# Optimization experiments

Measured on AMD Instinct MI355X. Metric: run time of the kernel, lower is better.

Reference implementation:

```python
import jax, jax.numpy as jnp
import numpy as np

N_NODES = 50000
N_EDGES = 800000
EDGE_DIM = 64
HID = 64


def setup_inputs() -> dict:
    key = jax.random.key(0)
    ks = jax.random.split(key, 8)
    hidden_atom_emb = jax.random.normal(ks[0], (N_NODES, HID), dtype=jnp.float32)
    edge_emb = jax.random.normal(ks[1], (N_EDGES, EDGE_DIM), dtype=jnp.float32)
    edge_list = jax.random.randint(ks[2], (N_EDGES, 2), 0, N_NODES, dtype=jnp.int64)
    # filter MLP params (xavier-uniform-like scaling)
    lim1 = float(np.sqrt(6.0 / (EDGE_DIM + HID)))
    W1 = jax.random.uniform(ks[3], (EDGE_DIM, HID), minval=-lim1, maxval=lim1, dtype=jnp.float32)
    b1 = jnp.zeros((HID,), dtype=jnp.float32)
    lim2 = float(np.sqrt(6.0 / (HID + HID)))
    W2 = jax.random.uniform(ks[4], (HID, HID), minval=-lim2, maxval=lim2, dtype=jnp.float32)
    b2 = jnp.zeros((HID,), dtype=jnp.float32)
    lim3 = 1.414 * float(np.sqrt(6.0 / (HID + 1)))
    linear_coef = jax.random.uniform(ks[5], (HID, 1), minval=-lim3, maxval=lim3, dtype=jnp.float32)
    return {
        'hidden_atom_emb': hidden_atom_emb,
        'edge_emb': edge_emb,
        'W1': W1, 'b1': b1, 'W2': W2, 'b2': b2,
        'linear_coef': linear_coef,
        'edge_list': edge_list,
    }


def reference(hidden_atom_emb, edge_emb, W1, b1, W2, b2, linear_coef, edge_list):
    # filter-generating MLP: Linear + tanh, Linear
    hidden_edge_emb = jnp.tanh(edge_emb @ W1 + b1) @ W2 + b2            # [E, H]
    # gather neighbor (source) embeddings and apply continuous filter
    msg = hidden_atom_emb[edge_list[:, 1]] * hidden_edge_emb           # [E, H]
    # unnormalized edge attention (scalar per edge)
    attn = jnp.exp(msg @ linear_coef)                                   # [E, 1]
    dest = edge_list[:, 0]
    n = hidden_atom_emb.shape[0]
    # scatter-sum over neighbors (dim=1 of the sparse [N,N,H] tensors)
    num = jax.ops.segment_sum(msg * attn, dest, num_segments=n)         # [N, H]
    den = jax.ops.segment_sum(jnp.broadcast_to(attn, msg.shape), dest, num_segments=n)  # [N, H]
    return jnp.where(den > 0, num / den, num)
```

## Files before the change

kernel.cpp:

```cpp
#include <hip/hip_runtime.h>
#include <math.h>


#define TE 64
#define HID 64

typedef __attribute__((ext_vector_type(8))) short short8;
typedef __attribute__((ext_vector_type(4))) float float4v;

__device__ __forceinline__ float fast_tanh(float x) {
    float t = __expf(2.0f * x);
    return 1.0f - 2.0f * __builtin_amdgcn_rcpf(t + 1.0f);
}

__device__ __forceinline__ void split_bf16(float x, unsigned short& hi,
                                           unsigned short& lo) {
    unsigned b = __float_as_uint(x);
    hi = (unsigned short)(b >> 16);
    float hf = __uint_as_float(b & 0xffff0000u);
    lo = (unsigned short)(__float_as_uint(x - hf) >> 16);
}

__global__ __launch_bounds__(256) void pack_w(
    const float* __restrict__ W1, const float* __restrict__ W2,
    unsigned short* __restrict__ wpack)
{
    int t = threadIdx.x;
    for (int i = 0; i < 16; ++i) {
        int idx = t * 16 + i;
        int k = idx >> 6, f = idx & 63;
        int nt = f >> 4, n = f & 15, ks = k >> 5, q = (k >> 3) & 3, j = k & 7;
        int fi = (((nt * 2 + ks) * 4 + q) * 16 + n) * 8 + j;
        unsigned short hi, lo;
        split_bf16(W1[idx], hi, lo);
        wpack[fi] = hi; wpack[4096 + fi] = lo;
        split_bf16(W2[idx], hi, lo);
        wpack[8192 + fi] = hi; wpack[12288 + fi] = lo;
    }
}


__global__ __launch_bounds__(256) void hist_kernel(
    const int2* __restrict__ edge_list, int* __restrict__ cursor, int E)
{
    int i = blockIdx.x * blockDim.x + threadIdx.x;
    if (i < E) atomicAdd(&cursor[edge_list[i].x], 1);
}

__global__ __launch_bounds__(1024) void scanA_kernel(
    int* __restrict__ a, int* __restrict__ blocksums, int N)
{
    __shared__ int wsum[16];
    const int t = threadIdx.x;
    const int lane = t & 63, wv = t >> 6;
    int i = blockIdx.x * 1024 + t;
    int x = (i < N) ? a[i] : 0;
    int v = x;
    #pragma unroll
    for (int d = 1; d < 64; d <<= 1) {
        int y = __shfl_up(v, d);
        if (lane >= d) v += y;
    }
    if (lane == 63) wsum[wv] = v;
    __syncthreads();
    if (wv == 0 && lane < 16) {
        int s = wsum[lane];
        #pragma unroll
        for (int d = 1; d < 16; d <<= 1) {
            int y = __shfl_up(s, d);
            if (lane >= d) s += y;
        }
        wsum[lane] = s;
    }
    __syncthreads();
    int incl = v + ((wv == 0) ? 0 : wsum[wv - 1]);
    if (i < N) a[i] = incl - x;
    if (t == 1023) blocksums[blockIdx.x] = incl;
}

__global__ __launch_bounds__(64) void scanB_kernel(int* __restrict__ bs, int nb)
{
    int lane = threadIdx.x;
    int x = (lane < nb) ? bs[lane] : 0;
    int v = x;
    #pragma unroll
    for (int d = 1; d < 64; d <<= 1) {
        int y = __shfl_up(v, d);
        if (lane >= d) v += y;
    }
    if (lane < nb) bs[lane] = v - x;
}

__global__ __launch_bounds__(1024) void scanC_kernel(
    int* __restrict__ a, const int* __restrict__ blocksums, int N)
{
    int i = blockIdx.x * 1024 + threadIdx.x;
    if (i < N) a[i] += blocksums[blockIdx.x];
}

__global__ __launch_bounds__(256) void perm_kernel(
    const int2* __restrict__ edge_list, int* __restrict__ cursor,
    int* __restrict__ perm, int E)
{
    int i = blockIdx.x * blockDim.x + threadIdx.x;
    if (i < E) {
        int d = edge_list[i].x;
        int p = atomicAdd(&cursor[d], 1);
        perm[p] = i;
    }
}


__global__ __launch_bounds__(256, 3) void edge_mlp_sorted(
    const float* __restrict__ atom,
    const float* __restrict__ edge_emb,
    const unsigned short* __restrict__ wpack,
    const float* __restrict__ b1,
    const float* __restrict__ b2,
    const float* __restrict__ coef,
    const int*   __restrict__ edge_list,
    const int*   __restrict__ perm,
    float* __restrict__ num,
    float* __restrict__ den,
    int E)
{
    __shared__ __align__(16) unsigned char SH[49152];
    __shared__ float b1s[HID], b2s[HID], cfs[HID];
    __shared__ float denacc[TE];
    __shared__ int   srcs[TE], pidx[TE], seg[TE], segdest[TE];
    __shared__ int   nseg_s, prevd_s, nextd_s;

    unsigned short* B1 = (unsigned short*)SH;
    unsigned short* B2 = (unsigned short*)(SH + 16384);
    unsigned short* A1 = (unsigned short*)(SH + 32768);
    float* H1  = (float*)(SH + 32768);
    float* ACC = (float*)SH;

    const int t    = threadIdx.x;
    const int eb   = blockIdx.x * TE;
    const int w    = t >> 6;
    const int lane = t & 63;
    const int q    = lane >> 4;
    const int n    = lane & 15;

    {
        const uint4* wp = (const uint4*)wpack;
        uint4* shw = (uint4*)SH;
        #pragma unroll
        for (int i = 0; i < 8; ++i)
            shw[t + 256 * i] = wp[t + 256 * i];
    }
    if (t < HID) { b1s[t] = b1[t]; b2s[t] = b2[t]; cfs[t] = coef[t]; }
    if (t < TE) {
        int eg = eb + t;
        if (eg >= E) eg = E - 1;
        pidx[t] = perm[eg];
    } else if (t == 64) {
        int pd = -1, nd = -1;
        if (eb > 0)      pd = edge_list[2 * perm[eb - 1]];
        if (eb + TE < E) nd = edge_list[2 * perm[eb + TE]];
        prevd_s = pd; nextd_s = nd;
    }
    __syncthreads();

    if (t < TE) {
        int e = pidx[t];
        int d = edge_list[2 * e + 0];
        int s = edge_list[2 * e + 1];
        srcs[t] = s;
        int dprev = __shfl_up(d, 1);
        int head = (t == 0 || dprev != d) ? 1 : 0;
        int sv = head;
        #pragma unroll
        for (int m = 1; m < 64; m <<= 1) {
            int y = __shfl_up(sv, m);
            if (t >= m) sv += y;
        }
        int sidx = sv - 1;
        seg[t] = sidx;
        if (head) segdest[sidx] = d;
        if (t == 63) nseg_s = sv;
    }
    {
        const int e = t >> 2, c = t & 3;
        const float* sp = edge_emb + (size_t)pidx[e] * HID + c * 16;
        float x[16];
        #pragma unroll
        for (int i = 0; i < 4; ++i) {
            float4 v = ((const float4*)sp)[i];
            x[4*i] = v.x; x[4*i+1] = v.y; x[4*i+2] = v.z; x[4*i+3] = v.w;
        }
        int wA = e >> 4, m = e & 15, ks = c >> 1;
        int cA = wA * 128 + ks * 64 + ((2 * c) & 3) * 16 + m;
        int cB = wA * 128 + ks * 64 + (((2 * c) & 3) + 1) * 16 + m;
        short8 hA, lA, hB, lB;
        #pragma unroll
        for (int j = 0; j < 8; ++j) {
            unsigned short hi, lo;
            split_bf16(x[j], hi, lo);
            hA[j] = (short)hi; lA[j] = (short)lo;
            split_bf16(x[8 + j], hi, lo);
            hB[j] = (short)hi; lB[j] = (short)lo;
        }
        *(short8*)&A1[cA * 8]        = hA;
        *(short8*)&A1[4096 + cA * 8] = lA;
        *(short8*)&A1[cB * 8]        = hB;
        *(short8*)&A1[4096 + cB * 8] = lB;
    }
    __syncthreads();

    float4v c1[4];
    #pragma unroll
    for (int i = 0; i < 4; ++i) c1[i] = (float4v){0.f, 0.f, 0.f, 0.f};
    {
        short8 ah0 = *(const short8*)&A1[(w * 128 + lane) * 8];
        short8 ah1 = *(const short8*)&A1[(w * 128 + 64 + lane) * 8];
        short8 al0 = *(const short8*)&A1[4096 + (w * 128 + lane) * 8];
        short8 al1 = *(const short8*)&A1[4096 + (w * 128 + 64 + lane) * 8];
        #pragma unroll
        for (int nt = 0; nt < 4; ++nt) {
            #pragma unroll
            for (int ks = 0; ks < 2; ++ks) {
                int cb = (nt * 2 + ks) * 64 + lane;
                short8 bh = *(const short8*)&B1[cb * 8];
                short8 bl = *(const short8*)&B1[4096 + cb * 8];
                short8 ah = ks ? ah1 : ah0;
                short8 al = ks ? al1 : al0;
                c1[nt] = __builtin_amdgcn_mfma_f32_16x16x32_bf16(ah, bh, c1[nt], 0, 0, 0);
                c1[nt] = __builtin_amdgcn_mfma_f32_16x16x32_bf16(ah, bl, c1[nt], 0, 0, 0);
                c1[nt] = __builtin_amdgcn_mfma_f32_16x16x32_bf16(al, bh, c1[nt], 0, 0, 0);
            }
        }
    }

    __syncthreads();

    {
        float* h1w = H1 + w * 1024;
        #pragma unroll
        for (int nt = 0; nt < 4; ++nt) {
            int f = nt * 16 + n;
            float bb = b1s[f];
            #pragma unroll
            for (int r = 0; r < 4; ++r) {
                int m = q * 4 + r;
                h1w[m * 64 + (f ^ ((m & 7) << 3))] = fast_tanh(c1[nt][r] + bb);
            }
        }
    }
    __syncthreads();

    {
        float4* az = (float4*)ACC;
        #pragma unroll
        for (int i = 0; i < 4; ++i)
            az[t + 256 * i] = (float4){0.f, 0.f, 0.f, 0.f};
        if (t < TE) denacc[t] = 0.f;
    }

    short8 a2h[2], a2l[2];
    {
        const float* h1w = H1 + w * 1024;
        int m = lane & 15;
        #pragma unroll
        for (int ks2 = 0; ks2 < 2; ++ks2) {
            int F0 = (ks2 * 32 + q * 8) ^ ((m & 7) << 3);
            const float* sp = h1w + m * 64 + F0;
            float4 u0 = *(const float4*)&sp[0];
            float4 u1 = *(const float4*)&sp[4];
            float xv[8] = {u0.x, u0.y, u0.z, u0.w, u1.x, u1.y, u1.z, u1.w};
            #pragma unroll
            for (int j = 0; j < 8; ++j) {
                unsigned short hi, lo;
                split_bf16(xv[j], hi, lo);
                a2h[ks2][j] = (short)hi; a2l[ks2][j] = (short)lo;
            }
        }
    }

    float4v c2[4];
    #pragma unroll
    for (int i = 0; i < 4; ++i) c2[i] = (float4v){0.f, 0.f, 0.f, 0.f};
    #pragma unroll
    for (int nt = 0; nt < 4; ++nt) {
        #pragma unroll
        for (int ks = 0; ks < 2; ++ks) {
            int cb = (nt * 2 + ks) * 64 + lane;
            short8 bh = *(const short8*)&B2[cb * 8];
            short8 bl = *(const short8*)&B2[4096 + cb * 8];
            c2[nt] = __builtin_amdgcn_mfma_f32_16x16x32_bf16(a2h[ks], bh, c2[nt], 0, 0, 0);
            c2[nt] = __builtin_amdgcn_mfma_f32_16x16x32_bf16(a2h[ks], bl, c2[nt], 0, 0, 0);
            c2[nt] = __builtin_amdgcn_mfma_f32_16x16x32_bf16(a2l[ks], bh, c2[nt], 0, 0, 0);
        }
    }

    float b2v[4], cfv[4];
    #pragma unroll
    for (int nt = 0; nt < 4; ++nt) {
        b2v[nt] = b2s[nt * 16 + n];
        cfv[nt] = cfs[nt * 16 + n];
    }
    float msg[4][4];
    float partial[4], at[4];
    #pragma unroll
    for (int r = 0; r < 4; ++r) {
        int s = srcs[w * 16 + q * 4 + r];
        const float* ap = atom + (size_t)s * HID + n;
        float p = 0.f;
        #pragma unroll
        for (int nt = 0; nt < 4; ++nt) {
            float hv = c2[nt][r] + b2v[nt];
            float av = ap[nt * 16];
            msg[r][nt] = av * hv;
            p = fmaf(msg[r][nt], cfv[nt], p);
        }
        partial[r] = p;
    }
    #pragma unroll
    for (int m = 1; m < 16; m <<= 1) {
        #pragma unroll
        for (int r = 0; r < 4; ++r)
            partial[r] += __shfl_xor(partial[r], m);
    }
    #pragma unroll
    for (int r = 0; r < 4; ++r) {
        int eg = eb + w * 16 + q * 4 + r;
        at[r] = (eg < E) ? __expf(partial[r]) : 0.f;
    }
    __syncthreads();

    {
        int e0L = w * 16 + q * 4;
        int curseg = seg[e0L];
        float a0 = msg[0][0] * at[0], a1 = msg[0][1] * at[0];
        float a2 = msg[0][2] * at[0], a3 = msg[0][3] * at[0];
        float rd = at[0];
        #pragma unroll
        for (int r = 1; r < 4; ++r) {
            int s2 = seg[e0L + r];
            if (s2 == curseg) {
                a0 = fmaf(msg[r][0], at[r], a0);
                a1 = fmaf(msg[r][1], at[r], a1);
                a2 = fmaf(msg[r][2], at[r], a2);
                a3 = fmaf(msg[r][3], at[r], a3);
                rd += at[r];
            } else {
                float* p = &ACC[curseg * 64 + n];
                atomicAdd(p + 0,  a0); atomicAdd(p + 16, a1);
                atomicAdd(p + 32, a2); atomicAdd(p + 48, a3);
                if (n == 0) atomicAdd(&denacc[curseg], rd);
                curseg = s2;
                a0 = msg[r][0] * at[r]; a1 = msg[r][1] * at[r];
                a2 = msg[r][2] * at[r]; a3 = msg[r][3] * at[r];
                rd = at[r];
            }
        }
        float* p = &ACC[curseg * 64 + n];
        atomicAdd(p + 0,  a0); atomicAdd(p + 16, a1);
        atomicAdd(p + 32, a2); atomicAdd(p + 48, a3);
        if (n == 0) atomicAdd(&denacc[curseg], rd);
    }
    __syncthreads();

    {
        int nseg = nseg_s;
        int s = t >> 2;
        int qq = t & 3;
        if (s < nseg) {
            int d = segdest[s];
            bool bnd = (s == 0 && d == prevd_s) ||
                       (s == nseg - 1 && d == nextd_s);
            float* np = num + (size_t)d * HID + qq * 16;
            const float* sp = &ACC[s * 64 + qq * 16];
            if (bnd) {
                #pragma unroll
                for (int j = 0; j < 16; ++j) atomicAdd(np + j, sp[j]);
                if (qq == 0) atomicAdd(&den[d], denacc[s]);
            } else {
                #pragma unroll
                for (int j = 0; j < 4; ++j)
                    ((float4*)np)[j] = *(const float4*)(sp + 4 * j);
                if (qq == 0) den[d] = denacc[s];
            }
        }
    }
}

__global__ __launch_bounds__(256) void finalize_kernel(
    float* __restrict__ out, const float* __restrict__ den, int n16)
{
    int i = blockIdx.x * blockDim.x + threadIdx.x;
    if (i >= n16) return;
    float d = den[i >> 4];
    if (d > 0.f) {
        float4* p = (float4*)out + i;
        float4 v = *p;
        float r = 1.0f / d;
        v.x *= r; v.y *= r; v.z *= r; v.w *= r;
        *p = v;
    }
}

extern "C" void kernel_launch(void* const* d_in, const int* in_sizes, int n_in,
                              void* d_out, int out_size, void* d_ws, size_t ws_size,
                              hipStream_t stream) {
    const float* atom      = (const float*)d_in[0];
    const float* edge_emb  = (const float*)d_in[1];
    const float* W1        = (const float*)d_in[2];
    const float* b1        = (const float*)d_in[3];
    const float* W2        = (const float*)d_in[4];
    const float* b2        = (const float*)d_in[5];
    const float* coef      = (const float*)d_in[6];
    const int*   edge_list = (const int*)d_in[7];

    const int N = in_sizes[0] / HID;
    const int E = in_sizes[1] / HID;

    float* den       = (float*)d_ws;
    int*   cursor    = (int*)d_ws + N;
    int*   blocksums = (int*)d_ws + 2 * N;
    int*   perm      = (int*)d_ws + 2 * N + 64;
    unsigned short* wpack = (unsigned short*)((int*)d_ws + 2 * N + 64 + E);

    hipMemsetAsync(d_out, 0, (size_t)N * HID * sizeof(float), stream);
    hipMemsetAsync(d_ws, 0, (size_t)(2 * N) * sizeof(int), stream);

    pack_w<<<1, 256, 0, stream>>>(W1, W2, wpack);

    int eblk = (E + 255) / 256;
    int nb   = (N + 1023) / 1024;
    hist_kernel<<<eblk, 256, 0, stream>>>((const int2*)edge_list, cursor, E);
    scanA_kernel<<<nb, 1024, 0, stream>>>(cursor, blocksums, N);
    scanB_kernel<<<1, 64, 0, stream>>>(blocksums, nb);
    scanC_kernel<<<nb, 1024, 0, stream>>>(cursor, blocksums, N);
    perm_kernel<<<eblk, 256, 0, stream>>>((const int2*)edge_list, cursor, perm, E);

    int nblk = (E + TE - 1) / TE;
    edge_mlp_sorted<<<nblk, 256, 0, stream>>>(
        atom, edge_emb, wpack, b1, b2, coef, edge_list, perm,
        (float*)d_out, den, E);

    int n16 = N * (HID / 4);
    finalize_kernel<<<(n16 + 255) / 256, 256, 0, stream>>>((float*)d_out, den, n16);
}
```

Before: 550.9 us.

## Make edge MLP kernel persistent with register prefetch of next tile

The edge MLP kernel becomes a persistent, grid-stride kernel over 64-edge tiles, with the grid capped at 768 blocks. Each block loads the packed weights into LDS once. It prefetches the next tile's perm entries, edge_list pairs and edge embeddings into registers while the current tile computes. The first-layer A fragments are now built directly in registers instead of being staged through LDS. The accumulator now shares the H1 buffer, is zeroed per tile, and several block-wide barriers are removed. The aims are to amortise weight loading and to hide gather latency. The cost is more register pressure and a more complex reuse of the LDS buffer.

```diff
diff --git a/kernel.cpp b/kernel.cpp
--- a/kernel.cpp
+++ b/kernel.cpp
@@ -4,6 +4,7 @@
 
 #define TE 64
 #define HID 64
+#define NBLK_MLP 768
 
 typedef __attribute__((ext_vector_type(8))) short short8;
 typedef __attribute__((ext_vector_type(4))) float float4v;
@@ -19,6 +20,17 @@
     hi = (unsigned short)(b >> 16);
     float hf = __uint_as_float(b & 0xffff0000u);
     lo = (unsigned short)(__float_as_uint(x - hf) >> 16);
+}
+
+__device__ __forceinline__ void split8(const float4 u0, const float4 u1,
+                                       short8& h, short8& l) {
+    float xv[8] = {u0.x, u0.y, u0.z, u0.w, u1.x, u1.y, u1.z, u1.w};
+    #pragma unroll
+    for (int j = 0; j < 8; ++j) {
+        unsigned short hi, lo;
+        split_bf16(xv[j], hi, lo);
+        h[j] = (short)hi; l[j] = (short)lo;
+    }
 }
 
 __global__ __launch_bounds__(256) void pack_w(
@@ -125,23 +137,21 @@
     int E)
 {
     __shared__ __align__(16) unsigned char SH[49152];
-    __shared__ float b1s[HID], b2s[HID], cfs[HID];
     __shared__ float denacc[TE];
-    __shared__ int   srcs[TE], pidx[TE], seg[TE], segdest[TE];
-    __shared__ int   nseg_s, prevd_s, nextd_s;
+    __shared__ int   segdest[TE];
 
     unsigned short* B1 = (unsigned short*)SH;
     unsigned short* B2 = (unsigned short*)(SH + 16384);
-    unsigned short* A1 = (unsigned short*)(SH + 32768);
     float* H1  = (float*)(SH + 32768);
-    float* ACC = (float*)SH;
+    float* ACC = H1;
 
     const int t    = threadIdx.x;
-    const int eb   = blockIdx.x * TE;
     const int w    = t >> 6;
     const int lane = t & 63;
     const int q    = lane >> 4;
     const int n    = lane & 15;
+    const int ntiles = (E + TE - 1) / TE;
+    const int stride = gridDim.x;
 
     {
         const uint4* wp = (const uint4*)wpack;
@@ -150,73 +160,93 @@
         for (int i = 0; i < 8; ++i)
             shw[t + 256 * i] = wp[t + 256 * i];
     }
-    if (t < HID) { b1s[t] = b1[t]; b2s[t] = b2[t]; cfs[t] = coef[t]; }
-    if (t < TE) {
-        int eg = eb + t;
-        if (eg >= E) eg = E - 1;
-        pidx[t] = perm[eg];
-    } else if (t == 64) {
-        int pd = -1, nd = -1;
-        if (eb > 0)      pd = edge_list[2 * perm[eb - 1]];
-        if (eb + TE < E) nd = edge_list[2 * perm[eb + TE]];
-        prevd_s = pd; nextd_s = nd;
+    float b1v[4], b2v[4], cfv[4];
+    #pragma unroll
+    for (int nt = 0; nt < 4; ++nt) {
+        b1v[nt] = b1[nt * 16 + n];
+        b2v[nt] = b2[nt * 16 + n];
+        cfv[nt] = coef[nt * 16 + n];
+    }
+    {
+        float4 z4 = {0.f, 0.f, 0.f, 0.f};
+        float4* az = (float4*)ACC;
+        #pragma unroll
+        for (int i = 0; i < 4; ++i) az[t + 256 * i] = z4;
+        if (t < TE) denacc[t] = 0.f;
     }
     __syncthreads();
 
-    if (t < TE) {
-        int e = pidx[t];
-        int d = edge_list[2 * e + 0];
-        int s = edge_list[2 * e + 1];
-        srcs[t] = s;
+    int tt = blockIdx.x;
+    int p_cur = 0, p_nxt = 0, p_nxt2 = 0;
+    int2 ds_cur = make_int2(0, 0), ds_nxt = make_int2(0, 0);
+    float4 rA0, rA1, rA2, rA3;
+    float4 rN0 = {0,0,0,0}, rN1 = {0,0,0,0}, rN2 = {0,0,0,0}, rN3 = {0,0,0,0};
+    {
+        int eg = tt * TE + lane; if (eg >= E) eg = E - 1;
+        p_cur = perm[eg];
+        ds_cur = ((const int2*)edge_list)[p_cur];
+        int pid = __shfl(p_cur, w * 16 + n);
+        const float* ep = edge_emb + (size_t)pid * HID;
+        rA0 = *(const float4*)(ep + q * 8);
+        rA1 = *(const float4*)(ep + q * 8 + 4);
+        rA2 = *(const float4*)(ep + 32 + q * 8);
+        rA3 = *(const float4*)(ep + 36 + q * 8);
+        int t2 = tt + stride;
+        if (t2 < ntiles) {
+            int eg2 = t2 * TE + lane; if (eg2 >= E) eg2 = E - 1;
+            p_nxt = perm[eg2];
+        }
+    }
+
+    for (; tt < ntiles; tt += stride) {
+        const int eb = tt * TE;
+        const bool hn = (tt + stride) < ntiles;
+
+        int d = ds_cur.x, s = ds_cur.y;
         int dprev = __shfl_up(d, 1);
-        int head = (t == 0 || dprev != d) ? 1 : 0;
+        int head = (lane == 0 || dprev != d) ? 1 : 0;
         int sv = head;
         #pragma unroll
         for (int m = 1; m < 64; m <<= 1) {
             int y = __shfl_up(sv, m);
-            if (t >= m) sv += y;
+            if (lane >= m) sv += y;
         }
         int sidx = sv - 1;
-        seg[t] = sidx;
-        if (head) segdest[sidx] = d;
-        if (t == 63) nseg_s = sv;
-    }
-    {
-        const int e = t >> 2, c = t & 3;
-        const float* sp = edge_emb + (size_t)pidx[e] * HID + c * 16;
-        float x[16];
-        #pragma unroll
-        for (int i = 0; i < 4; ++i) {
-            float4 v = ((const float4*)sp)[i];
-            x[4*i] = v.x; x[4*i+1] = v.y; x[4*i+2] = v.z; x[4*i+3] = v.w;
-        }
-        int wA = e >> 4, m = e & 15, ks = c >> 1;
-        int cA = wA * 128 + ks * 64 + ((2 * c) & 3) * 16 + m;
-        int cB = wA * 128 + ks * 64 + (((2 * c) & 3) + 1) * 16 + m;
-        short8 hA, lA, hB, lB;
-        #pragma unroll
-        for (int j = 0; j < 8; ++j) {
-            unsigned short hi, lo;
-            split_bf16(x[j], hi, lo);
-            hA[j] = (short)hi; lA[j] = (short)lo;
-            split_bf16(x[8 + j], hi, lo);
-            hB[j] = (short)hi; lB[j] = (short)lo;
-        }
-        *(short8*)&A1[cA * 8]        = hA;
-        *(short8*)&A1[4096 + cA * 8] = lA;
-        *(short8*)&A1[cB * 8]        = hB;
-        *(short8*)&A1[4096 + cB * 8] = lB;
-    }
-    __syncthreads();
-
-    float4v c1[4];
-    #pragma unroll
-    for (int i = 0; i < 4; ++i) c1[i] = (float4v){0.f, 0.f, 0.f, 0.f};
-    {
-        short8 ah0 = *(const short8*)&A1[(w * 128 + lane) * 8];
-        short8 ah1 = *(const short8*)&A1[(w * 128 + 64 + lane) * 8];
-        short8 al0 = *(const short8*)&A1[4096 + (w * 128 + lane) * 8];
-        short8 al1 = *(const short8*)&A1[4096 + (w * 128 + 64 + lane) * 8];
+        int nseg = __shfl(sv, 63);
+
+        int pdnd = -1;
+        if (lane == 0 && eb > 0)        pdnd = edge_list[2 * perm[eb - 1]];
+        if (lane == 63 && eb + TE < E)  pdnd = edge_list[2 * perm[eb + TE]];
+
+        int seg_r[4], src_r[4];
+        #pragma unroll
+        for (int r = 0; r < 4; ++r) {
+            int el = w * 16 + q * 4 + r;
+            seg_r[r] = __shfl(sidx, el);
+            src_r[r] = __shfl(s, el);
+        }
+
+        if (hn) {
+            ds_nxt = ((const int2*)edge_list)[p_nxt];
+            int pid2 = __shfl(p_nxt, w * 16 + n);
+            const float* ep2 = edge_emb + (size_t)pid2 * HID;
+            rN0 = *(const float4*)(ep2 + q * 8);
+            rN1 = *(const float4*)(ep2 + q * 8 + 4);
+            rN2 = *(const float4*)(ep2 + 32 + q * 8);
+            rN3 = *(const float4*)(ep2 + 36 + q * 8);
+            int t3 = tt + 2 * stride;
+            if (t3 < ntiles) {
+                int eg3 = t3 * TE + lane; if (eg3 >= E) eg3 = E - 1;
+                p_nxt2 = perm[eg3];
+            }
+        }
+
+        short8 a1h[2], a1l[2];
+        split8(rA0, rA1, a1h[0], a1l[0]);
+        split8(rA2, rA3, a1h[1], a1l[1]);
+        float4v c1[4];
+        #pragma unroll
+        for (int i = 0; i < 4; ++i) c1[i] = (float4v){0.f, 0.f, 0.f, 0.f};
         #pragma unroll
         for (int nt = 0; nt < 4; ++nt) {
             #pragma unroll
@@ -224,164 +254,155 @@
                 int cb = (nt * 2 + ks) * 64 + lane;
                 short8 bh = *(const short8*)&B1[cb * 8];
                 short8 bl = *(const short8*)&B1[4096 + cb * 8];
-                short8 ah = ks ? ah1 : ah0;
-                short8 al = ks ? al1 : al0;
-                c1[nt] = __builtin_amdgcn_mfma_f32_16x16x32_bf16(ah, bh, c1[nt], 0, 0, 0);
-                c1[nt] = __builtin_amdgcn_mfma_f32_16x16x32_bf16(ah, bl, c1[nt], 0, 0, 0);
-                c1[nt] = __builtin_amdgcn_mfma_f32_16x16x32_bf16(al, bh, c1[nt], 0, 0, 0);
-            }
-        }
-    }
-
-    __syncthreads();
-
-    {
+                c1[nt] = __builtin_amdgcn_mfma_f32_16x16x32_bf16(a1h[ks], bh, c1[nt], 0, 0, 0);
+                c1[nt] = __builtin_amdgcn_mfma_f32_16x16x32_bf16(a1h[ks], bl, c1[nt], 0, 0, 0);
+                c1[nt] = __builtin_amdgcn_mfma_f32_16x16x32_bf16(a1l[ks], bh, c1[nt], 0, 0, 0);
+            }
+        }
+
+        float av[4][4];
+        #pragma unroll
+        for (int r = 0; r < 4; ++r) {
+            const float* ap = atom + (size_t)src_r[r] * HID + n;
+            #pragma unroll
+            for (int nt = 0; nt < 4; ++nt) av[r][nt] = ap[nt * 16];
+        }
+
         float* h1w = H1 + w * 1024;
         #pragma unroll
         for (int nt = 0; nt < 4; ++nt) {
             int f = nt * 16 + n;
-            float bb = b1s[f];
             #pragma unroll
             for (int r = 0; r < 4; ++r) {
                 int m = q * 4 + r;
-                h1w[m * 64 + (f ^ ((m & 7) << 3))] = fast_tanh(c1[nt][r] + bb);
-            }
-        }
-    }
-    __syncthreads();
-
-    {
-        float4* az = (float4*)ACC;
-        #pragma unroll
-        for (int i = 0; i < 4; ++i)
-            az[t + 256 * i] = (float4){0.f, 0.f, 0.f, 0.f};
-        if (t < TE) denacc[t] = 0.f;
-    }
-
-    short8 a2h[2], a2l[2];
-    {
-        const float* h1w = H1 + w * 1024;
-        int m = lane & 15;
-        #pragma unroll
-        for (int ks2 = 0; ks2 < 2; ++ks2) {
-            int F0 = (ks2 * 32 + q * 8) ^ ((m & 7) << 3);
-            const float* sp = h1w + m * 64 + F0;
-            float4 u0 = *(const float4*)&sp[0];
-            float4 u1 = *(const float4*)&sp[4];
-            float xv[8] = {u0.x, u0.y, u0.z, u0.w, u1.x, u1.y, u1.z, u1.w};
-            #pragma unroll
-            for (int j = 0; j < 8; ++j) {
-                unsigned short hi, lo;
-                split_bf16(xv[j], hi, lo);
-                a2h[ks2][j] = (short)hi; a2l[ks2][j] = (short)lo;
-            }
-        }
-    }
-
-    float4v c2[4];
-    #pragma unroll
-    for (int i = 0; i < 4; ++i) c2[i] = (float4v){0.f, 0.f, 0.f, 0.f};
-    #pragma unroll
-    for (int nt = 0; nt < 4; ++nt) {
-        #pragma unroll
-        for (int ks = 0; ks < 2; ++ks) {
-            int cb = (nt * 2 + ks) * 64 + lane;
-            short8 bh = *(const short8*)&B2[cb * 8];
-            short8 bl = *(const short8*)&B2[4096 + cb * 8];
-            c2[nt] = __builtin_amdgcn_mfma_f32_16x16x32_bf16(a2h[ks], bh, c2[nt], 0, 0, 0);
-            c2[nt] = __builtin_amdgcn_mfma_f32_16x16x32_bf16(a2h[ks], bl, c2[nt], 0, 0, 0);
-            c2[nt] = __builtin_amdgcn_mfma_f32_16x16x32_bf16(a2l[ks], bh, c2[nt], 0, 0, 0);
-        }
-    }
-
-    float b2v[4], cfv[4];
-    #pragma unroll
-    for (int nt = 0; nt < 4; ++nt) {
-        b2v[nt] = b2s[nt * 16 + n];
-        cfv[nt] = cfs[nt * 16 + n];
-    }
-    float msg[4][4];
-    float partial[4], at[4];
-    #pragma unroll
-    for (int r = 0; r < 4; ++r) {
-        int s = srcs[w * 16 + q * 4 + r];
-        const float* ap = atom + (size_t)s * HID + n;
-        float p = 0.f;
+                h1w[m * 64 + (f ^ ((m & 7) << 3))] = fast_tanh(c1[nt][r] + b1v[nt]);
+            }
+        }
+        asm volatile("s_waitcnt lgkmcnt(0)" ::: "memory");
+
+        short8 a2h[2], a2l[2];
+        {
+            int m = n;
+            #pragma unroll
+            for (int ks2 = 0; ks2 < 2; ++ks2) {
+                int F0 = (ks2 * 32 + q * 8) ^ ((m & 7) << 3);
+                const float* sp = h1w + m * 64 + F0;
+                float4 u0 = *(const float4*)&sp[0];
+                float4 u1 = *(const float4*)&sp[4];
+                split8(u0, u1, a2h[ks2], a2l[ks2]);
+            }
+        }
+        {
+            float4 z4 = {0.f, 0.f, 0.f, 0.f};
+            float* zp = h1w + lane * 16;
+            #pragma unroll
+            for (int i = 0; i < 4; ++i) *(float4*)(zp + 4 * i) = z4;
+        }
+
+        float4v c2[4];
+        #pragma unroll
+        for (int i = 0; i < 4; ++i) c2[i] = (float4v){0.f, 0.f, 0.f, 0.f};
         #pragma unroll
         for (int nt = 0; nt < 4; ++nt) {
-            float hv = c2[nt][r] + b2v[nt];
-            float av = ap[nt * 16];
-            msg[r][nt] = av * hv;
-            p = fmaf(msg[r][nt], cfv[nt], p);
-        }
-        partial[r] = p;
-    }
-    #pragma unroll
-    for (int m = 1; m < 16; m <<= 1) {
-        #pragma unroll
-        for (int r = 0; r < 4; ++r)
-            partial[r] += __shfl_xor(partial[r], m);
-    }
-    #pragma unroll
-    for (int r = 0; r < 4; ++r) {
-        int eg = eb + w * 16 + q * 4 + r;
-        at[r] = (eg < E) ? __expf(partial[r]) : 0.f;
-    }
-    __syncthreads();
-
-    {
-        int e0L = w * 16 + q * 4;
-        int curseg = seg[e0L];
-        float a0 = msg[0][0] * at[0], a1 = msg[0][1] * at[0];
-        float a2 = msg[0][2] * at[0], a3 = msg[0][3] * at[0];
-        float rd = at[0];
-        #pragma unroll
-        for (int r = 1; r < 4; ++r) {
-            int s2 = seg[e0L + r];
-            if (s2 == curseg) {
-                a0 = fmaf(msg[r][0], at[r], a0);
-                a1 = fmaf(msg[r][1], at[r], a1);
-                a2 = fmaf(msg[r][2], at[r], a2);
-                a3 = fmaf(msg[r][3], at[r], a3);
-                rd += at[r];
-            } else {
-                float* p = &ACC[curseg * 64 + n];
-                atomicAdd(p + 0,  a0); atomicAdd(p + 16, a1);
-                atomicAdd(p + 32, a2); atomicAdd(p + 48, a3);
-                if (n == 0) atomicAdd(&denacc[curseg], rd);
-                curseg = s2;
-                a0 = msg[r][0] * at[r]; a1 = msg[r][1] * at[r];
-                a2 = msg[r][2] * at[r]; a3 = msg[r][3] * at[r];
-                rd = at[r];
-            }
-        }
-        float* p = &ACC[curseg * 64 + n];
-        atomicAdd(p + 0,  a0); atomicAdd(p + 16, a1);
-        atomicAdd(p + 32, a2); atomicAdd(p + 48, a3);
-        if (n == 0) atomicAdd(&denacc[curseg], rd);
-    }
-    __syncthreads();
-
-    {
-        int nseg = nseg_s;
-        int s = t >> 2;
-        int qq = t & 3;
-        if (s < nseg) {
-            int d = segdest[s];
-            bool bnd = (s == 0 && d == prevd_s) ||
-                       (s == nseg - 1 && d == nextd_s);
-            float* np = num + (size_t)d * HID + qq * 16;
-            const float* sp = &ACC[s * 64 + qq * 16];
-            if (bnd) {
-                #pragma unroll
-                for (int j = 0; j < 16; ++j) atomicAdd(np + j, sp[j]);
-                if (qq == 0) atomicAdd(&den[d], denacc[s]);
-            } else {
-                #pragma unroll
-                for (int j = 0; j < 4; ++j)
-                    ((float4*)np)[j] = *(const float4*)(sp + 4 * j);
-                if (qq == 0) den[d] = denacc[s];
-            }
+            #pragma unroll
+            for (int ks = 0; ks < 2; ++ks) {
+                int cb = (nt * 2 + ks) * 64 + lane;
+                short8 bh = *(const short8*)&B2[cb * 8];
+                short8 bl = *(const short8*)&B2[4096 + cb * 8];
+                c2[nt] = __builtin_amdgcn_mfma_f32_16x16x32_bf16(a2h[ks], bh, c2[nt], 0, 0, 0);
+                c2[nt] = __builtin_amdgcn_mfma_f32_16x16x32_bf16(a2h[ks], bl, c2[nt], 0, 0, 0);
+                c2[nt] = __builtin_amdgcn_mfma_f32_16x16x32_bf16(a2l[ks], bh, c2[nt], 0, 0, 0);
+            }
+        }
+
+        float msg[4][4], partial[4], at[4];
+        #pragma unroll
+        for (int r = 0; r < 4; ++r) {
+            float p = 0.f;
+            #pragma unroll
+            for (int nt = 0; nt < 4; ++nt) {
+                float hv = c2[nt][r] + b2v[nt];
+                msg[r][nt] = av[r][nt] * hv;
+                p = fmaf(msg[r][nt], cfv[nt], p);
+            }
+            partial[r] = p;
+        }
+        #pragma unroll
+        for (int m = 1; m < 16; m <<= 1) {
+            #pragma unroll
+            for (int r = 0; r < 4; ++r)
+                partial[r] += __shfl_xor(partial[r], m);
+        }
+        #pragma unroll
+        for (int r = 0; r < 4; ++r) {
+            int eg = eb + w * 16 + q * 4 + r;
+            at[r] = (eg < E) ? __expf(partial[r]) : 0.f;
+        }
+
+        __syncthreads();
+
+        if (head) segdest[sidx] = d;
+
+        {
+            int curseg = seg_r[0];
+            float acc0 = msg[0][0] * at[0], acc1 = msg[0][1] * at[0];
+            float acc2 = msg[0][2] * at[0], acc3 = msg[0][3] * at[0];
+            float rd = at[0];
+            #pragma unroll
+            for (int r = 1; r < 4; ++r) {
+                if (seg_r[r] == curseg) {
+                    acc0 = fmaf(msg[r][0], at[r], acc0);
+                    acc1 = fmaf(msg[r][1], at[r], acc1);
+                    acc2 = fmaf(msg[r][2], at[r], acc2);
+                    acc3 = fmaf(msg[r][3], at[r], acc3);
+                    rd += at[r];
+                } else {
+                    float* p = &ACC[curseg * 64 + n];
+                    atomicAdd(p + 0,  acc0); atomicAdd(p + 16, acc1);
+                    atomicAdd(p + 32, acc2); atomicAdd(p + 48, acc3);
+                    if (n == 0) atomicAdd(&denacc[curseg], rd);
+                    curseg = seg_r[r];
+                    acc0 = msg[r][0] * at[r]; acc1 = msg[r][1] * at[r];
+                    acc2 = msg[r][2] * at[r]; acc3 = msg[r][3] * at[r];
+                    rd = at[r];
+                }
+            }
+            float* p = &ACC[curseg * 64 + n];
+            atomicAdd(p + 0,  acc0); atomicAdd(p + 16, acc1);
+            atomicAdd(p + 32, acc2); atomicAdd(p + 48, acc3);
+            if (n == 0) atomicAdd(&denacc[curseg], rd);
+        }
+        __syncthreads();
+
+        {
+            int prevd = __shfl(pdnd, 0);
+            int nextd = __shfl(pdnd, 63);
+            int sg = t >> 2;
+            int qq = t & 3;
+            if (sg < nseg) {
+                int d2 = segdest[sg];
+                bool bnd = (sg == 0 && d2 == prevd) ||
+                           (sg == nseg - 1 && d2 == nextd);
+                float* np = num + (size_t)d2 * HID + qq * 16;
+                const float* sp = &ACC[sg * 64 + qq * 16];
+                if (bnd) {
+                    #pragma unroll
+                    for (int j = 0; j < 16; ++j) atomicAdd(np + j, sp[j]);
+                    if (qq == 0) { atomicAdd(&den[d2], denacc[sg]); denacc[sg] = 0.f; }
+                } else {
+                    #pragma unroll
+                    for (int j = 0; j < 4; ++j)
+                        ((float4*)np)[j] = *(const float4*)(sp + 4 * j);
+                    if (qq == 0) { den[d2] = denacc[sg]; denacc[sg] = 0.f; }
+                }
+            }
+        }
+        __syncthreads();
+
+        if (hn) {
+            ds_cur = ds_nxt;
+            rA0 = rN0; rA1 = rN1; rA2 = rN2; rA3 = rN3;
+            p_nxt = p_nxt2;
         }
     }
 }
@@ -435,7 +456,8 @@
     scanC_kernel<<<nb, 1024, 0, stream>>>(cursor, blocksums, N);
     perm_kernel<<<eblk, 256, 0, stream>>>((const int2*)edge_list, cursor, perm, E);
 
-    int nblk = (E + TE - 1) / TE;
+    int ntl  = (E + TE - 1) / TE;
+    int nblk = ntl < NBLK_MLP ? ntl : NBLK_MLP;
     edge_mlp_sorted<<<nblk, 256, 0, stream>>>(
         atom, edge_emb, wpack, b1, b2, coef, edge_list, perm,
         (float*)d_out, den, E);
```

New measurement: 524.8 us. 1.05x faster.
